# Kernel tuning notes

Measured on AMD Instinct MI355X. Metric: run time of the kernel, lower is better.

The kernel has to match this reference:

```python
import jax, jax.numpy as jnp
import numpy as np

N, F_DIM, H_DIM = 8192, 128, 128

def setup_inputs() -> dict:
    key = jax.random.key(0)
    ks = jax.random.split(key, 7)
    inp = {
        "input": jax.random.normal(ks[0], (N, F_DIM), dtype=jnp.float32),
        "wavelets": jax.random.normal(ks[1], (N, N), dtype=jnp.float32) / np.sqrt(N),
        "wavelets_inv": jax.random.normal(ks[2], (N, N), dtype=jnp.float32) / np.sqrt(N),
        # layer 1 params
        "W1": jax.random.uniform(ks[3], (F_DIM, H_DIM), dtype=jnp.float32,
                                 minval=-np.sqrt(6.0/(F_DIM+H_DIM)), maxval=np.sqrt(6.0/(F_DIM+H_DIM))),
        "f1": jax.random.uniform(ks[4], (N,), dtype=jnp.float32, minval=0.9, maxval=1.1),
        # layer 2 params
        "W2": jax.random.uniform(ks[5], (H_DIM, H_DIM), dtype=jnp.float32,
                                 minval=-np.sqrt(6.0/(H_DIM+H_DIM)), maxval=np.sqrt(6.0/(H_DIM+H_DIM))),
        "f2": jax.random.uniform(ks[6], (N,), dtype=jnp.float32, minval=0.9, maxval=1.1),
    }
    return inp

def _gwnn_layer(features, wavelets, wavelets_inv, W, filt):
    # torch: wavelets @ diag(filt) @ (wavelets_inv @ (features @ W))
    # diag(filt) matmul == column-wise scale of wavelets (broadcast elementwise)
    xw = features @ W                      # [N, out]
    spec = wavelets_inv @ xw               # [N, out] spectral-domain features
    spec = filt[:, None] * spec            # apply learnable diagonal filter
    return wavelets @ spec                 # [N, out]

def reference(input, wavelets, wavelets_inv, W1, f1, W2, f2):
    # eval mode: dropout is identity
    h1 = jax.nn.relu(_gwnn_layer(input, wavelets, wavelets_inv, W1, f1))
    out = _gwnn_layer(h1, wavelets, wavelets_inv, W2, f2)
    return out
```

## Files before the change

kernel.cpp:

```cpp
#include <hip/hip_runtime.h>
#include <hip/hip_bf16.h>
#include <stdint.h>


typedef __attribute__((ext_vector_type(4))) float f32x4;
typedef __attribute__((ext_vector_type(8))) short s16x8;
typedef __attribute__((ext_vector_type(4))) short s16x4;

#define DEVI static __device__ __forceinline__

DEVI short bf1(float x){ __bf16 h = (__bf16)x; return __builtin_bit_cast(short, h); }

DEVI s16x8 cvt8(f32x4 lo, f32x4 hi){
  s16x8 r;
#pragma unroll
  for (int i = 0; i < 4; ++i){ r[i] = bf1(lo[i]); r[4+i] = bf1(hi[i]); }
  return r;
}

DEVI void glds16(const void* g, void* l){
  __builtin_amdgcn_global_load_lds((const __attribute__((address_space(1))) void*)g,
                                   (__attribute__((address_space(3))) void*)l, 16, 0, 0);
}

template<int N> DEVI void waitvm(){
  if constexpr (N == 0)      asm volatile("s_waitcnt vmcnt(0)" ::: "memory");
  else if constexpr (N == 5) asm volatile("s_waitcnt vmcnt(5)" ::: "memory");
  else if constexpr (N == 6) asm volatile("s_waitcnt vmcnt(6)" ::: "memory");
}

__global__ __launch_bounds__(256, 2) void gemm_sk(
    const float* __restrict__ Ap, const short* __restrict__ Btp,
    float* __restrict__ Pp, int K, int M)
{
  constexpr int BM = 32, BN = 128, BK = 64;
  constexpr int ASZ = BM*BK*4;
  constexpr int BSZ = BN*BK*2;
  constexpr int TSZ = ASZ + BSZ;
  constexpr int NL  = 6;
  constexpr int NBUF = 3, PRE = 2;
  __shared__ uint8_t lds[NBUF*TSZ];

  const int tid  = threadIdx.x;
  const int lane = tid & 63;
  const int wv   = tid >> 6;
  const int la   = lane & 15;
  const int g4   = lane >> 4;
  const int m0   = blockIdx.x * BM;
  const int kh   = blockIdx.y;
  const int K2   = K >> 1;
  const size_t kb = (size_t)kh * K2;

  const float* Af = Ap;
  int r0 = (wv<<3) + (lane>>4);
  int r1 = r0 + 4;
  const float* gA0 = Af + (size_t)(m0+r0)*K + kb + (((lane&15)^(r0&15))<<2);
  const float* gA1 = Af + (size_t)(m0+r1)*K + kb + (((lane&15)^(r1&15))<<2);
  const int nb0 = (wv<<5) + (lane>>3);
  const short* gB0 = Btp + (size_t)(nb0    )*K + kb + (((lane&7)^(nb0&7))<<3);
  const short* gB1 = Btp + (size_t)(nb0+ 8 )*K + kb + (((lane&7)^(nb0&7))<<3);
  const short* gB2 = Btp + (size_t)(nb0+16 )*K + kb + (((lane&7)^(nb0&7))<<3);
  const short* gB3 = Btp + (size_t)(nb0+24 )*K + kb + (((lane&7)^(nb0&7))<<3);

  int aoff[2][2][2];
  int boff[2][2];
#pragma unroll
  for (int mi = 0; mi < 2; ++mi){
    const int r = mi*16 + la;
#pragma unroll
    for (int kf = 0; kf < 2; ++kf){
      const int v0 = kf*8 + (g4<<1);
      aoff[mi][kf][0] = r*256 + (((v0  )^(r&15))<<4);
      aoff[mi][kf][1] = r*256 + (((v0+1)^(r&15))<<4);
    }
  }
#pragma unroll
  for (int ni = 0; ni < 2; ++ni){
    const int n = (wv<<5) + ni*16 + la;
#pragma unroll
    for (int kf = 0; kf < 2; ++kf){
      const int u = kf*4 + g4;
      boff[ni][kf] = n*128 + ((u^(n&7))<<4);
    }
  }

  f32x4 acc[2][2] = {};

  auto STAGE = [&](uint8_t* buf){
    uint8_t* Ab = buf;
    uint8_t* Bb = buf + ASZ;
    glds16(gA0, Ab + (wv<<11));
    glds16(gA1, Ab + (wv<<11) + 1024);
    gA0 += BK; gA1 += BK;
    glds16(gB0, Bb + (wv<<12));
    glds16(gB1, Bb + (wv<<12) + 1024);
    glds16(gB2, Bb + (wv<<12) + 2048);
    glds16(gB3, Bb + (wv<<12) + 3072);
    gB0 += BK; gB1 += BK; gB2 += BK; gB3 += BK;
  };

  auto COMPUTE = [&](const uint8_t* buf){
    const uint8_t* Ab = buf;
    const uint8_t* Bb = buf + ASZ;
#pragma unroll
    for (int kf = 0; kf < 2; ++kf){
      s16x8 a0 = cvt8(*(const f32x4*)(Ab + aoff[0][kf][0]), *(const f32x4*)(Ab + aoff[0][kf][1]));
      s16x8 a1 = cvt8(*(const f32x4*)(Ab + aoff[1][kf][0]), *(const f32x4*)(Ab + aoff[1][kf][1]));
      s16x8 b0 = *(const s16x8*)(Bb + boff[0][kf]);
      s16x8 b1 = *(const s16x8*)(Bb + boff[1][kf]);
      acc[0][0] = __builtin_amdgcn_mfma_f32_16x16x32_bf16(a0, b0, acc[0][0], 0, 0, 0);
      acc[0][1] = __builtin_amdgcn_mfma_f32_16x16x32_bf16(a0, b1, acc[0][1], 0, 0, 0);
      acc[1][0] = __builtin_amdgcn_mfma_f32_16x16x32_bf16(a1, b0, acc[1][0], 0, 0, 0);
      acc[1][1] = __builtin_amdgcn_mfma_f32_16x16x32_bf16(a1, b1, acc[1][1], 0, 0, 0);
    }
  };

  const int nsteps = K2 >> 6;
  uint8_t* const lend = lds + NBUF*TSZ;
  uint8_t* bs = lds;
  uint8_t* bc = lds;
  for (int s = 0; s < PRE && s < nsteps; ++s){
    STAGE(bs);
    bs += TSZ; if (bs == lend) bs = lds;
  }
  for (int t = 0; t < nsteps; ++t){
    if (t < nsteps - 1) waitvm<NL>();
    else                waitvm<0>();
    __builtin_amdgcn_s_barrier();
    asm volatile("" ::: "memory");
    if (t + PRE < nsteps){
      STAGE(bs);
      bs += TSZ; if (bs == lend) bs = lds;
    }
    COMPUTE(bc);
    bc += TSZ; if (bc == lend) bc = lds;
    asm volatile("" ::: "memory");
  }

  float* P = Pp + (size_t)kh * M * 128;
  const int mbase = m0 + (g4<<2);
  const int nc0   = (wv<<5) + la;
#pragma unroll
  for (int mi = 0; mi < 2; ++mi)
#pragma unroll
    for (int ni = 0; ni < 2; ++ni)
#pragma unroll
      for (int r = 0; r < 4; ++r)
        P[(size_t)(mbase + (mi<<4) + r)*128 + nc0 + (ni<<4)] = acc[mi][ni][r];
}

template<bool ABF>
__global__ __launch_bounds__(256, 1) void gemm_k(
    const void* __restrict__ Ap, const short* __restrict__ Btp,
    void* __restrict__ Outp, int K, int M)
{
  constexpr int BM = 32, BN = 128, BK = 64;
  constexpr int ASZ = ABF ? BM*BK*2 : BM*BK*4;
  constexpr int BSZ = BN*BK*2;
  constexpr int TSZ = ASZ + BSZ;
  constexpr int NL  = ABF ? 5 : 6;
  constexpr int NBUF = 3, PRE = 2;
  __shared__ uint8_t lds[NBUF*TSZ];

  const int tid  = threadIdx.x;
  const int lane = tid & 63;
  const int wv   = tid >> 6;
  const int la   = lane & 15;
  const int g4   = lane >> 4;
  const int m0   = blockIdx.x * BM;

  const float* gA0 = nullptr; const float* gA1 = nullptr; const short* gAh = nullptr;
  if constexpr (!ABF){
    const float* Af = (const float*)Ap;
    int r0 = (wv<<3) + (lane>>4);
    int r1 = r0 + 4;
    gA0 = Af + (size_t)(m0+r0)*K + (((lane&15)^(r0&15))<<2);
    gA1 = Af + (size_t)(m0+r1)*K + (((lane&15)^(r1&15))<<2);
  } else {
    const short* Ah = (const short*)Ap;
    int r = (wv<<3) + (lane>>3);
    gAh = Ah + (size_t)(m0+r)*K + (((lane&7)^(r&7))<<3);
  }
  const int nb0 = (wv<<5) + (lane>>3);
  const short* gB0 = Btp + (size_t)(nb0    )*K + (((lane&7)^(nb0&7))<<3);
  const short* gB1 = Btp + (size_t)(nb0+ 8 )*K + (((lane&7)^(nb0&7))<<3);
  const short* gB2 = Btp + (size_t)(nb0+16 )*K + (((lane&7)^(nb0&7))<<3);
  const short* gB3 = Btp + (size_t)(nb0+24 )*K + (((lane&7)^(nb0&7))<<3);

  int aoff[2][2][2];
  int boff[2][2];
#pragma unroll
  for (int mi = 0; mi < 2; ++mi){
    const int r = mi*16 + la;
#pragma unroll
    for (int kf = 0; kf < 2; ++kf){
      if constexpr (!ABF){
        const int v0 = kf*8 + (g4<<1);
        aoff[mi][kf][0] = r*256 + (((v0  )^(r&15))<<4);
        aoff[mi][kf][1] = r*256 + (((v0+1)^(r&15))<<4);
      } else {
        const int u = kf*4 + g4;
        aoff[mi][kf][0] = r*128 + ((u^(r&7))<<4);
        aoff[mi][kf][1] = 0;
      }
    }
  }
#pragma unroll
  for (int ni = 0; ni < 2; ++ni){
    const int n = (wv<<5) + ni*16 + la;
#pragma unroll
    for (int kf = 0; kf < 2; ++kf){
      const int u = kf*4 + g4;
      boff[ni][kf] = n*128 + ((u^(n&7))<<4);
    }
  }

  f32x4 acc[2][2] = {};

  auto STAGE = [&](uint8_t* buf){
    uint8_t* Ab = buf;
    uint8_t* Bb = buf + ASZ;
    if constexpr (!ABF){
      glds16(gA0, Ab + (wv<<11));
      glds16(gA1, Ab + (wv<<11) + 1024);
      gA0 += BK; gA1 += BK;
    } else {
      glds16(gAh, Ab + (wv<<10));
      gAh += BK;
    }
    glds16(gB0, Bb + (wv<<12));
    glds16(gB1, Bb + (wv<<12) + 1024);
    glds16(gB2, Bb + (wv<<12) + 2048);
    glds16(gB3, Bb + (wv<<12) + 3072);
    gB0 += BK; gB1 += BK; gB2 += BK; gB3 += BK;
  };

  auto COMPUTE = [&](const uint8_t* buf){
    const uint8_t* Ab = buf;
    const uint8_t* Bb = buf + ASZ;
#pragma unroll
    for (int kf = 0; kf < 2; ++kf){
      s16x8 a0, a1, b0, b1;
      if constexpr (!ABF){
        a0 = cvt8(*(const f32x4*)(Ab + aoff[0][kf][0]), *(const f32x4*)(Ab + aoff[0][kf][1]));
        a1 = cvt8(*(const f32x4*)(Ab + aoff[1][kf][0]), *(const f32x4*)(Ab + aoff[1][kf][1]));
      } else {
        a0 = *(const s16x8*)(Ab + aoff[0][kf][0]);
        a1 = *(const s16x8*)(Ab + aoff[1][kf][0]);
      }
      b0 = *(const s16x8*)(Bb + boff[0][kf]);
      b1 = *(const s16x8*)(Bb + boff[1][kf]);
      acc[0][0] = __builtin_amdgcn_mfma_f32_16x16x32_bf16(a0, b0, acc[0][0], 0, 0, 0);
      acc[0][1] = __builtin_amdgcn_mfma_f32_16x16x32_bf16(a0, b1, acc[0][1], 0, 0, 0);
      acc[1][0] = __builtin_amdgcn_mfma_f32_16x16x32_bf16(a1, b0, acc[1][0], 0, 0, 0);
      acc[1][1] = __builtin_amdgcn_mfma_f32_16x16x32_bf16(a1, b1, acc[1][1], 0, 0, 0);
    }
  };

  const int nsteps = K >> 6;
  uint8_t* const lend = lds + NBUF*TSZ;
  uint8_t* bs = lds;
  uint8_t* bc = lds;
  for (int s = 0; s < PRE && s < nsteps; ++s){
    STAGE(bs);
    bs += TSZ; if (bs == lend) bs = lds;
  }
  for (int t = 0; t < nsteps; ++t){
    if (t < nsteps - 1) waitvm<NL>();
    else                waitvm<0>();
    __builtin_amdgcn_s_barrier();
    asm volatile("" ::: "memory");
    if (t + PRE < nsteps){
      STAGE(bs);
      bs += TSZ; if (bs == lend) bs = lds;
    }
    COMPUTE(bc);
    bc += TSZ; if (bc == lend) bc = lds;
    asm volatile("" ::: "memory");
  }

  const int mbase = m0 + (g4<<2);
  const int nc0   = (wv<<5) + la;
#pragma unroll
  for (int mi = 0; mi < 2; ++mi){
#pragma unroll
    for (int ni = 0; ni < 2; ++ni){
      s16x4 pk;
#pragma unroll
      for (int r = 0; r < 4; ++r) pk[r] = bf1(acc[mi][ni][r]);
      *(s16x4*)((short*)Outp + (size_t)(nc0 + (ni<<4))*M + (mbase + (mi<<4))) = pk;
    }
  }
}


__global__ __launch_bounds__(256) void red_t(
    const float* __restrict__ Pp, const float* __restrict__ fp,
    short* __restrict__ out, int M)
{
  __shared__ short t[128*65];
  const float* P0 = Pp;
  const float* P1 = Pp + (size_t)M*128;
  const int m0 = blockIdx.x * 64;
  const int tid = threadIdx.x;
#pragma unroll
  for (int it = 0; it < 8; ++it){
    const int idx = it*256 + tid;
    const int m = idx >> 5, nq = idx & 31;
    f32x4 a = ((const f32x4*)(P0 + (size_t)(m0+m)*128))[nq];
    f32x4 b = ((const f32x4*)(P1 + (size_t)(m0+m)*128))[nq];
    const float fv = fp[m0+m];
#pragma unroll
    for (int j = 0; j < 4; ++j)
      t[(nq*4+j)*65 + m] = bf1(fv * (a[j] + b[j]));
  }
  __syncthreads();
#pragma unroll
  for (int it = 0; it < 8; ++it){
    const int idx = it*256 + tid;
    const int n = idx >> 4, mc = idx & 15;
    s16x4 v;
#pragma unroll
    for (int j = 0; j < 4; ++j) v[j] = t[n*65 + mc*4 + j];
    *(s16x4*)(out + (size_t)n*M + m0 + mc*4) = v;
  }
}

__global__ __launch_bounds__(256) void red_r(
    const float* __restrict__ Pp, short* __restrict__ out, int M)
{
  const float* P0 = Pp;
  const float* P1 = Pp + (size_t)M*128;
  const size_t i0 = (size_t)(blockIdx.x*256 + threadIdx.x) * 8;
  f32x4 a0 = ((const f32x4*)(P0 + i0))[0], a1 = ((const f32x4*)(P0 + i0))[1];
  f32x4 b0 = ((const f32x4*)(P1 + i0))[0], b1 = ((const f32x4*)(P1 + i0))[1];
  s16x8 v;
#pragma unroll
  for (int j = 0; j < 4; ++j){
    v[j]   = bf1(fmaxf(a0[j] + b0[j], 0.0f));
    v[4+j] = bf1(fmaxf(a1[j] + b1[j], 0.0f));
  }
  *(s16x8*)(out + i0) = v;
}

__global__ __launch_bounds__(256) void red_f(
    const float* __restrict__ Pp, float* __restrict__ out, int M)
{
  const float* P0 = Pp;
  const float* P1 = Pp + (size_t)M*128;
  const size_t i0 = (size_t)(blockIdx.x*256 + threadIdx.x) * 4;
  f32x4 a = *(const f32x4*)(P0 + i0);
  f32x4 b = *(const f32x4*)(P1 + i0);
  *(f32x4*)(out + i0) = a + b;
}

__global__ void wtrans_k(const float* __restrict__ W1, const float* __restrict__ W2,
                         short* __restrict__ T1, short* __restrict__ T2){
  const int idx = blockIdx.x*256 + threadIdx.x;
  const int m = idx >> 14, rem = idx & 16383;
  const int n = rem >> 7, k = rem & 127;
  const float* W = m ? W2 : W1;
  short* T = m ? T2 : T1;
  T[n*128 + k] = bf1(W[k*128 + n]);
}

extern "C" void kernel_launch(void* const* d_in, const int* in_sizes, int n_in,
                              void* d_out, int out_size, void* d_ws, size_t ws_size,
                              hipStream_t stream){
  const float* input = (const float*)d_in[0];
  const float* wav   = (const float*)d_in[1];
  const float* winv  = (const float*)d_in[2];
  const float* W1    = (const float*)d_in[3];
  const float* f1    = (const float*)d_in[4];
  const float* W2    = (const float*)d_in[5];
  const float* f2    = (const float*)d_in[6];

  uint8_t* ws = (uint8_t*)d_ws;
  short* W1T = (short*)(ws);
  short* W2T = (short*)(ws + (32<<10));
  short* XWT = (short*)(ws + (64<<10));
  short* SPT = (short*)(ws + (64<<10) + (2<<20));
  short* H1  = (short*)(ws + (64<<10) + (4<<20));
  float* P   = (float*)(ws + (64<<10) + (6<<20));

  constexpr int M = 8192;
  dim3 b(256);
  dim3 gsk(M/32, 2);
  dim3 gns(M/32);
  dim3 grt(M/64);
  dim3 grr(M*128/(256*8));
  dim3 grf(M*128/(256*4));
  dim3 gt(128);

  wtrans_k<<<gt, b, 0, stream>>>(W1, W2, W1T, W2T);
  gemm_k<false><<<gns, b, 0, stream>>>(input, W1T, XWT, 128, M);
  gemm_sk<<<gsk, b, 0, stream>>>(winv, XWT, P, M, M);
  red_t  <<<grt, b, 0, stream>>>(P, f1, SPT, M);
  gemm_sk<<<gsk, b, 0, stream>>>(wav, SPT, P, M, M);
  red_r  <<<grr, b, 0, stream>>>(P, H1, M);
  gemm_k<true ><<<gns, b, 0, stream>>>(H1, W2T, XWT, 128, M);
  gemm_sk<<<gsk, b, 0, stream>>>(winv, XWT, P, M, M);
  red_t  <<<grt, b, 0, stream>>>(P, f2, SPT, M);
  gemm_sk<<<gsk, b, 0, stream>>>(wav, SPT, P, M, M);
  red_f  <<<grf, b, 0, stream>>>(P, (float*)d_out, M);
}
```

Before: 346.9 us.

## Enlarge big-GEMM tile to 128x128 and split K four ways

Replaces the 32-row, 2-way split-K kernel for the N×N GEMMs with a 128×128 tile. Each wave now computes 32 rows against all 128 columns, and K is split four ways. This raises MFMA work per LDS fragment load and cuts redundant B-tile fetches. The reduction kernels now sum four partial buffers instead of two. The cost is more partial-sum traffic, a larger workspace, higher register and LDS use, and only one block per CU.

```diff
diff --git a/kernel.cpp b/kernel.cpp
--- a/kernel.cpp
+++ b/kernel.cpp
@@ -24,20 +24,20 @@
 }
 
 template<int N> DEVI void waitvm(){
-  if constexpr (N == 0)      asm volatile("s_waitcnt vmcnt(0)" ::: "memory");
-  else if constexpr (N == 5) asm volatile("s_waitcnt vmcnt(5)" ::: "memory");
-  else if constexpr (N == 6) asm volatile("s_waitcnt vmcnt(6)" ::: "memory");
-}
-
-__global__ __launch_bounds__(256, 2) void gemm_sk(
+  if constexpr (N == 0)       asm volatile("s_waitcnt vmcnt(0)"  ::: "memory");
+  else if constexpr (N == 5)  asm volatile("s_waitcnt vmcnt(5)"  ::: "memory");
+  else if constexpr (N == 6)  asm volatile("s_waitcnt vmcnt(6)"  ::: "memory");
+  else if constexpr (N == 12) asm volatile("s_waitcnt vmcnt(12)" ::: "memory");
+}
+
+__global__ __launch_bounds__(256, 1) void gemm_big(
     const float* __restrict__ Ap, const short* __restrict__ Btp,
     float* __restrict__ Pp, int K, int M)
 {
-  constexpr int BM = 32, BN = 128, BK = 64;
+  constexpr int BM = 128, BK = 64;
   constexpr int ASZ = BM*BK*4;
-  constexpr int BSZ = BN*BK*2;
+  constexpr int BSZ = 128*BK*2;
   constexpr int TSZ = ASZ + BSZ;
-  constexpr int NL  = 6;
   constexpr int NBUF = 3, PRE = 2;
   __shared__ uint8_t lds[NBUF*TSZ];
 
@@ -47,15 +47,18 @@
   const int la   = lane & 15;
   const int g4   = lane >> 4;
   const int m0   = blockIdx.x * BM;
-  const int kh   = blockIdx.y;
-  const int K2   = K >> 1;
-  const size_t kb = (size_t)kh * K2;
-
-  const float* Af = Ap;
-  int r0 = (wv<<3) + (lane>>4);
-  int r1 = r0 + 4;
-  const float* gA0 = Af + (size_t)(m0+r0)*K + kb + (((lane&15)^(r0&15))<<2);
-  const float* gA1 = Af + (size_t)(m0+r1)*K + kb + (((lane&15)^(r1&15))<<2);
+  const int kq   = blockIdx.y;
+  const int K4   = K >> 2;
+  const int kb   = kq * K4;
+
+  const float* gAbase = Ap + (size_t)m0*K + kb;
+  int aoffg[8];
+#pragma unroll
+  for (int j = 0; j < 8; ++j){
+    const int rl = (wv<<5) + (j<<2) + (lane>>4);
+    aoffg[j] = rl*K + (((lane&15) ^ (rl&15))<<2);
+  }
+
   const int nb0 = (wv<<5) + (lane>>3);
   const short* gB0 = Btp + (size_t)(nb0    )*K + kb + (((lane&7)^(nb0&7))<<3);
   const short* gB1 = Btp + (size_t)(nb0+ 8 )*K + kb + (((lane&7)^(nb0&7))<<3);
@@ -63,10 +66,9 @@
   const short* gB3 = Btp + (size_t)(nb0+24 )*K + kb + (((lane&7)^(nb0&7))<<3);
 
   int aoff[2][2][2];
-  int boff[2][2];
 #pragma unroll
   for (int mi = 0; mi < 2; ++mi){
-    const int r = mi*16 + la;
+    const int r = (wv<<5) + mi*16 + la;
 #pragma unroll
     for (int kf = 0; kf < 2; ++kf){
       const int v0 = kf*8 + (g4<<1);
@@ -74,9 +76,10 @@
       aoff[mi][kf][1] = r*256 + (((v0+1)^(r&15))<<4);
     }
   }
-#pragma unroll
-  for (int ni = 0; ni < 2; ++ni){
-    const int n = (wv<<5) + ni*16 + la;
+  int boff[8][2];
+#pragma unroll
+  for (int ni = 0; ni < 8; ++ni){
+    const int n = ni*16 + la;
 #pragma unroll
     for (int kf = 0; kf < 2; ++kf){
       const int u = kf*4 + g4;
@@ -84,73 +87,73 @@
     }
   }
 
-  f32x4 acc[2][2] = {};
-
-  auto STAGE = [&](uint8_t* buf){
-    uint8_t* Ab = buf;
-    uint8_t* Bb = buf + ASZ;
-    glds16(gA0, Ab + (wv<<11));
-    glds16(gA1, Ab + (wv<<11) + 1024);
-    gA0 += BK; gA1 += BK;
+  f32x4 acc[2][8] = {};
+
+  int kk = 0;
+  uint8_t* const lend = lds + NBUF*TSZ;
+  uint8_t* bs = lds;
+  uint8_t* bc = lds;
+
+  auto STAGE = [&](){
+    uint8_t* Ab = bs;
+    uint8_t* Bb = bs + ASZ;
+#pragma unroll
+    for (int j = 0; j < 8; ++j)
+      glds16(gAbase + aoffg[j] + kk, Ab + (wv<<13) + (j<<10));
+    kk += BK;
     glds16(gB0, Bb + (wv<<12));
     glds16(gB1, Bb + (wv<<12) + 1024);
     glds16(gB2, Bb + (wv<<12) + 2048);
     glds16(gB3, Bb + (wv<<12) + 3072);
     gB0 += BK; gB1 += BK; gB2 += BK; gB3 += BK;
+    bs += TSZ; if (bs == lend) bs = lds;
   };
 
-  auto COMPUTE = [&](const uint8_t* buf){
-    const uint8_t* Ab = buf;
-    const uint8_t* Bb = buf + ASZ;
-#pragma unroll
-    for (int kf = 0; kf < 2; ++kf){
-      s16x8 a0 = cvt8(*(const f32x4*)(Ab + aoff[0][kf][0]), *(const f32x4*)(Ab + aoff[0][kf][1]));
-      s16x8 a1 = cvt8(*(const f32x4*)(Ab + aoff[1][kf][0]), *(const f32x4*)(Ab + aoff[1][kf][1]));
-      s16x8 b0 = *(const s16x8*)(Bb + boff[0][kf]);
-      s16x8 b1 = *(const s16x8*)(Bb + boff[1][kf]);
-      acc[0][0] = __builtin_amdgcn_mfma_f32_16x16x32_bf16(a0, b0, acc[0][0], 0, 0, 0);
-      acc[0][1] = __builtin_amdgcn_mfma_f32_16x16x32_bf16(a0, b1, acc[0][1], 0, 0, 0);
-      acc[1][0] = __builtin_amdgcn_mfma_f32_16x16x32_bf16(a1, b0, acc[1][0], 0, 0, 0);
-      acc[1][1] = __builtin_amdgcn_mfma_f32_16x16x32_bf16(a1, b1, acc[1][1], 0, 0, 0);
-    }
+  auto COMPUTE = [&](){
+    const uint8_t* Ab = bc;
+    const uint8_t* Bb = bc + ASZ;
+#pragma unroll
+    for (int kf = 0; kf < 2; ++kf){
+      s16x8 a0 = cvt8(*(const f32x4*)(Ab + aoff[0][kf][0]),
+                      *(const f32x4*)(Ab + aoff[0][kf][1]));
+      s16x8 a1 = cvt8(*(const f32x4*)(Ab + aoff[1][kf][0]),
+                      *(const f32x4*)(Ab + aoff[1][kf][1]));
+#pragma unroll
+      for (int ni = 0; ni < 8; ++ni){
+        s16x8 b = *(const s16x8*)(Bb + boff[ni][kf]);
+        acc[0][ni] = __builtin_amdgcn_mfma_f32_16x16x32_bf16(a0, b, acc[0][ni], 0, 0, 0);
+        acc[1][ni] = __builtin_amdgcn_mfma_f32_16x16x32_bf16(a1, b, acc[1][ni], 0, 0, 0);
+      }
+    }
+    bc += TSZ; if (bc == lend) bc = lds;
   };
 
-  const int nsteps = K2 >> 6;
-  uint8_t* const lend = lds + NBUF*TSZ;
-  uint8_t* bs = lds;
-  uint8_t* bc = lds;
-  for (int s = 0; s < PRE && s < nsteps; ++s){
-    STAGE(bs);
-    bs += TSZ; if (bs == lend) bs = lds;
-  }
-  for (int t = 0; t < nsteps; ++t){
-    if (t < nsteps - 1) waitvm<NL>();
-    else                waitvm<0>();
+  const int ns = K4 >> 6;
+  for (int s = 0; s < PRE && s < ns; ++s) STAGE();
+
+  for (int t = 0; t < ns; ++t){
+    if (t < ns - 1) waitvm<12>();
+    else            waitvm<0>();
     __builtin_amdgcn_s_barrier();
     asm volatile("" ::: "memory");
-    if (t + PRE < nsteps){
-      STAGE(bs);
-      bs += TSZ; if (bs == lend) bs = lds;
-    }
-    COMPUTE(bc);
-    bc += TSZ; if (bc == lend) bc = lds;
+    if (t + PRE < ns) STAGE();
+    COMPUTE();
     asm volatile("" ::: "memory");
   }
 
-  float* P = Pp + (size_t)kh * M * 128;
-  const int mbase = m0 + (g4<<2);
-  const int nc0   = (wv<<5) + la;
+  float* P = Pp + (size_t)kq * M * 128;
+  const int rbase = m0 + (wv<<5) + (g4<<2);
 #pragma unroll
   for (int mi = 0; mi < 2; ++mi)
 #pragma unroll
-    for (int ni = 0; ni < 2; ++ni)
+    for (int ni = 0; ni < 8; ++ni)
 #pragma unroll
       for (int r = 0; r < 4; ++r)
-        P[(size_t)(mbase + (mi<<4) + r)*128 + nc0 + (ni<<4)] = acc[mi][ni][r];
+        P[(size_t)(rbase + mi*16 + r)*128 + ni*16 + la] = acc[mi][ni][r];
 }
 
 template<bool ABF>
-__global__ __launch_bounds__(256, 1) void gemm_k(
+__global__ __launch_bounds__(256, 1) void sgemm(
     const void* __restrict__ Ap, const short* __restrict__ Btp,
     void* __restrict__ Outp, int K, int M)
 {
@@ -257,20 +260,19 @@
     }
   };
 
-  const int nsteps = K >> 6;
+  const int ns = K >> 6;
   uint8_t* const lend = lds + NBUF*TSZ;
   uint8_t* bs = lds;
   uint8_t* bc = lds;
-  for (int s = 0; s < PRE && s < nsteps; ++s){
+  for (int s = 0; s < PRE && s < ns; ++s){
     STAGE(bs);
     bs += TSZ; if (bs == lend) bs = lds;
   }
-  for (int t = 0; t < nsteps; ++t){
-    if (t < nsteps - 1) waitvm<NL>();
-    else                waitvm<0>();
+  for (int t = 0; t < ns; ++t){
+    if (t < ns - 1) waitvm<NL>(); else waitvm<0>();
     __builtin_amdgcn_s_barrier();
     asm volatile("" ::: "memory");
-    if (t + PRE < nsteps){
+    if (t + PRE < ns){
       STAGE(bs);
       bs += TSZ; if (bs == lend) bs = lds;
     }
@@ -299,20 +301,22 @@
     short* __restrict__ out, int M)
 {
   __shared__ short t[128*65];
-  const float* P0 = Pp;
-  const float* P1 = Pp + (size_t)M*128;
+  const size_t S = (size_t)M*128;
   const int m0 = blockIdx.x * 64;
   const int tid = threadIdx.x;
 #pragma unroll
   for (int it = 0; it < 8; ++it){
     const int idx = it*256 + tid;
     const int m = idx >> 5, nq = idx & 31;
-    f32x4 a = ((const f32x4*)(P0 + (size_t)(m0+m)*128))[nq];
-    f32x4 b = ((const f32x4*)(P1 + (size_t)(m0+m)*128))[nq];
+    const float* base = Pp + (size_t)(m0+m)*128;
+    f32x4 a = ((const f32x4*)(base      ))[nq];
+    f32x4 b = ((const f32x4*)(base +   S))[nq];
+    f32x4 c = ((const f32x4*)(base + 2*S))[nq];
+    f32x4 d = ((const f32x4*)(base + 3*S))[nq];
     const float fv = fp[m0+m];
 #pragma unroll
     for (int j = 0; j < 4; ++j)
-      t[(nq*4+j)*65 + m] = bf1(fv * (a[j] + b[j]));
+      t[(nq*4+j)*65 + m] = bf1(fv * ((a[j] + b[j]) + (c[j] + d[j])));
   }
   __syncthreads();
 #pragma unroll
@@ -329,16 +333,18 @@
 __global__ __launch_bounds__(256) void red_r(
     const float* __restrict__ Pp, short* __restrict__ out, int M)
 {
-  const float* P0 = Pp;
-  const float* P1 = Pp + (size_t)M*128;
+  const size_t S = (size_t)M*128;
   const size_t i0 = (size_t)(blockIdx.x*256 + threadIdx.x) * 8;
-  f32x4 a0 = ((const f32x4*)(P0 + i0))[0], a1 = ((const f32x4*)(P0 + i0))[1];
-  f32x4 b0 = ((const f32x4*)(P1 + i0))[0], b1 = ((const f32x4*)(P1 + i0))[1];
   s16x8 v;
 #pragma unroll
-  for (int j = 0; j < 4; ++j){
-    v[j]   = bf1(fmaxf(a0[j] + b0[j], 0.0f));
-    v[4+j] = bf1(fmaxf(a1[j] + b1[j], 0.0f));
+  for (int h = 0; h < 2; ++h){
+    f32x4 a = *(const f32x4*)(Pp + i0 + 4*h);
+    f32x4 b = *(const f32x4*)(Pp + i0 + 4*h + S);
+    f32x4 c = *(const f32x4*)(Pp + i0 + 4*h + 2*S);
+    f32x4 d = *(const f32x4*)(Pp + i0 + 4*h + 3*S);
+#pragma unroll
+    for (int j = 0; j < 4; ++j)
+      v[4*h+j] = bf1(fmaxf((a[j] + b[j]) + (c[j] + d[j]), 0.0f));
   }
   *(s16x8*)(out + i0) = v;
 }
@@ -346,12 +352,13 @@
 __global__ __launch_bounds__(256) void red_f(
     const float* __restrict__ Pp, float* __restrict__ out, int M)
 {
-  const float* P0 = Pp;
-  const float* P1 = Pp + (size_t)M*128;
+  const size_t S = (size_t)M*128;
   const size_t i0 = (size_t)(blockIdx.x*256 + threadIdx.x) * 4;
-  f32x4 a = *(const f32x4*)(P0 + i0);
-  f32x4 b = *(const f32x4*)(P1 + i0);
-  *(f32x4*)(out + i0) = a + b;
+  f32x4 a = *(const f32x4*)(Pp + i0);
+  f32x4 b = *(const f32x4*)(Pp + i0 + S);
+  f32x4 c = *(const f32x4*)(Pp + i0 + 2*S);
+  f32x4 d = *(const f32x4*)(Pp + i0 + 3*S);
+  *(f32x4*)(out + i0) = (a + b) + (c + d);
 }
 
 __global__ void wtrans_k(const float* __restrict__ W1, const float* __restrict__ W2,
@@ -375,6 +382,7 @@
   const float* W2    = (const float*)d_in[5];
   const float* f2    = (const float*)d_in[6];
 
+  constexpr int M = 8192;
   uint8_t* ws = (uint8_t*)d_ws;
   short* W1T = (short*)(ws);
   short* W2T = (short*)(ws + (32<<10));
@@ -383,9 +391,8 @@
   short* H1  = (short*)(ws + (64<<10) + (4<<20));
   float* P   = (float*)(ws + (64<<10) + (6<<20));
 
-  constexpr int M = 8192;
   dim3 b(256);
-  dim3 gsk(M/32, 2);
+  dim3 gbig(M/128, 4);
   dim3 gns(M/32);
   dim3 grt(M/64);
   dim3 grr(M*128/(256*8));
@@ -393,14 +400,14 @@
   dim3 gt(128);
 
   wtrans_k<<<gt, b, 0, stream>>>(W1, W2, W1T, W2T);
-  gemm_k<false><<<gns, b, 0, stream>>>(input, W1T, XWT, 128, M);
-  gemm_sk<<<gsk, b, 0, stream>>>(winv, XWT, P, M, M);
+  sgemm<false><<<gns, b, 0, stream>>>(input, W1T, XWT, 128, M);
+  gemm_big<<<gbig, b, 0, stream>>>(winv, XWT, P, M, M);
   red_t  <<<grt, b, 0, stream>>>(P, f1, SPT, M);
-  gemm_sk<<<gsk, b, 0, stream>>>(wav, SPT, P, M, M);
+  gemm_big<<<gbig, b, 0, stream>>>(wav, SPT, P, M, M);
   red_r  <<<grr, b, 0, stream>>>(P, H1, M);
-  gemm_k<true ><<<gns, b, 0, stream>>>(H1, W2T, XWT, 128, M);
-  gemm_sk<<<gsk, b, 0, stream>>>(winv, XWT, P, M, M);
+  sgemm<true ><<<gns, b, 0, stream>>>(H1, W2T, XWT, 128, M);
+  gemm_big<<<gbig, b, 0, stream>>>(winv, XWT, P, M, M);
   red_t  <<<grt, b, 0, stream>>>(P, f2, SPT, M);
-  gemm_sk<<<gsk, b, 0, stream>>>(wav, SPT, P, M, M);
+  gemm_big<<<gbig, b, 0, stream>>>(wav, SPT, P, M, M);
   red_f  <<<grf, b, 0, stream>>>(P, (float*)d_out, M);
 }
```

Measured after the change: 306.9 us. -11.5%, faster.
